# Kernel tuning notes

Hardware: AMD Instinct MI355X
Metric: run time of the kernel (lower is better)

The kernel has to match this reference:

```python
import jax, jax.numpy as jnp
import numpy as np

N, D_IN, H, D_OUT = 32, 1024, 2048, 256
P = H * D_IN + H + D_OUT * H + D_OUT  # flattened params per network
SCALE = 4e-4  # ~1/sqrt(2P): keeps pairwise ||diff||^2 = O(1) so exp(-d/2) doesn't underflow
EPS = 0.1     # step size used in optimize()


def setup_inputs() -> dict:
    key = jax.random.key(0)
    k1, k2, k3, k4, k5, k6 = jax.random.split(key, 6)
    return {
        "W1": jax.random.normal(k1, (N, H, D_IN), jnp.float32) * SCALE,
        "b1": jax.random.normal(k2, (N, H), jnp.float32) * SCALE,
        "W2": jax.random.normal(k3, (N, D_OUT, H), jnp.float32) * SCALE,
        "b2": jax.random.normal(k4, (N, D_OUT), jnp.float32) * SCALE,
        "X": jax.random.normal(k5, (4096, D_IN), jnp.float32),
        "y": jax.random.normal(k6, (4096, D_OUT), jnp.float32),
    }


def reference(W1, b1, W2, b2, X, y):
    # One SVGD iteration (do_one_iteration with eps=0.1), vectorized over the
    # ensemble. Faithful to the source's actual math:
    #   dlogp_i = d/dz log_prior + d/dz log_prior = -2*theta_i   (likelihood grad
    #   is computed but discarded in derivative_log_posterior_compute, so X, y
    #   do not affect the update)
    #   kd(i,j) = exp(-||theta_i - theta_j||^2 / 2),  dkd_i = -kd*(theta_i-theta_j)
    #   phi_i = (1/n) * sum_{j=1..n-1} [ kd(i,j)*dlogp_i + dkd(i,j) ]
    #         = (1/n) * ( -3*S_i*theta_i + sum_{j>=1} kd(i,j)*theta_j ),  S_i = sum_{j>=1} kd(i,j)
    #   theta_i <- theta_i + eps*phi_i
    n = W1.shape[0]
    theta = jnp.concatenate(
        [W1.reshape(n, -1), b1, W2.reshape(n, -1), b2], axis=1
    )  # [n, P]
    sq = jnp.sum(theta * theta, axis=1)                      # [n]
    d2 = sq[:, None] + sq[None, :] - 2.0 * (theta @ theta.T)  # [n, n] squared dists
    K = jnp.exp(-0.5 * jnp.maximum(d2, 0.0))                  # RBF kernel, sigma=1
    Kj = K[:, 1:]                                             # loop runs j = 1..n-1
    S = jnp.sum(Kj, axis=1)                                   # [n]
    phi = (-3.0 * S[:, None] * theta + Kj @ theta[1:]) / n    # [n, P]
    return theta + EPS * phi
```

## Files before the change

### kernel.cpp

```cpp
#include <hip/hip_runtime.h>
#include <hip/hip_bf16.h>
#include <stdint.h>

#define NP     32
#define P_W1   2097152
#define P_B1   2048
#define P_W2   524288
#define P_B2   256
#define OFFB1  2097152
#define OFFW2  2099200
#define OFFB2  2623488
#define P_TOT  2623744
#define EPS_F  0.1f

typedef short  bf16x8 __attribute__((ext_vector_type(8)));
typedef float  f32x16 __attribute__((ext_vector_type(16)));

__device__ __forceinline__ short f2bf(float x) {
    uint32_t u = __builtin_bit_cast(uint32_t, x);
    u += 0x7fffu + ((u >> 16) & 1u);
    return (short)(u >> 16);
}

struct Seg { const float* p; int stride; int off; };

__device__ __forceinline__ Seg seg_of(const float* W1, const float* b1,
                                      const float* W2, const float* b2, int pbase) {
    Seg s;
    if (pbase < OFFB1)      { s.p = W1; s.stride = P_W1; s.off = pbase; }
    else if (pbase < OFFW2) { s.p = b1; s.stride = P_B1; s.off = pbase - OFFB1; }
    else if (pbase < OFFB2) { s.p = W2; s.stride = P_W2; s.off = pbase - OFFW2; }
    else                    { s.p = b2; s.stride = P_B2; s.off = pbase - OFFB2; }
    return s;
}

__global__ void zero_kernel(float* __restrict__ G) {
    G[threadIdx.x] = 0.0f;
}

__global__ void __launch_bounds__(256)
gram_kernel(const float* __restrict__ W1, const float* __restrict__ b1,
            const float* __restrict__ W2, const float* __restrict__ b2,
            float* __restrict__ G) {
    const int lane   = threadIdx.x & 63;
    const int wave   = (blockIdx.x * 256 + threadIdx.x) >> 6;
    const int nwaves = gridDim.x * 4;
    const int row    = lane & 31;
    const int q      = lane >> 5;

    f32x16 acc;
    #pragma unroll
    for (int r = 0; r < 16; r++) acc[r] = 0.0f;

    for (int c = wave; c < P_TOT / 64; c += nwaves) {
        const int kb = c * 64;
        Seg s = seg_of(W1, b1, W2, b2, kb);
        const float* base = s.p + (size_t)row * s.stride + s.off + q * 8;

        float v[4][8];
        #pragma unroll
        for (int cc = 0; cc < 4; cc++) {
            const float4 lo = *reinterpret_cast<const float4*>(base + cc * 16);
            const float4 hi = *reinterpret_cast<const float4*>(base + cc * 16 + 4);
            v[cc][0] = lo.x; v[cc][1] = lo.y; v[cc][2] = lo.z; v[cc][3] = lo.w;
            v[cc][4] = hi.x; v[cc][5] = hi.y; v[cc][6] = hi.z; v[cc][7] = hi.w;
        }
        #pragma unroll
        for (int cc = 0; cc < 4; cc++) {
            bf16x8 f;
            #pragma unroll
            for (int e = 0; e < 8; e++) f[e] = f2bf(v[cc][e]);
            acc = __builtin_amdgcn_mfma_f32_32x32x16_bf16(f, f, acc, 0, 0, 0);
        }
    }

    #pragma unroll
    for (int r = 0; r < 16; r++) {
        const int orow = (r & 3) + 8 * (r >> 2) + 4 * q;
        atomicAdd(&G[orow * 32 + row], acc[r]);
    }
}

__global__ void computeM_kernel(const float* __restrict__ G, float* __restrict__ Mp) {
    __shared__ float Ks[32][32];
    const int t = threadIdx.x;
    const int i = t >> 5, j = t & 31;
    const float sqi = G[i * 33];
    const float sqj = G[j * 33];
    const float d2  = fmaxf(sqi + sqj - 2.0f * G[i * 32 + j], 0.0f);
    const float K   = expf(-0.5f * d2);
    Ks[i][j] = K;
    __syncthreads();
    float S = 0.0f;
    for (int m = 1; m < 32; m++) S += Ks[i][m];
    float v = (j >= 1) ? (EPS_F / 32.0f) * K : 0.0f;
    if (i == j) v -= (3.0f * EPS_F / 32.0f) * S;
    Mp[i * 32 + j] = v;
}

__global__ void __launch_bounds__(256)
apply_kernel(const float* __restrict__ W1, const float* __restrict__ b1,
             const float* __restrict__ W2, const float* __restrict__ b2,
             const float* __restrict__ Mp, float* __restrict__ out) {
    const int lane   = threadIdx.x & 63;
    const int wave   = (blockIdx.x * 256 + threadIdx.x) >> 6;
    const int nwaves = gridDim.x * 4;
    const int col    = lane & 31;
    const int q      = lane >> 5;

    bf16x8 a0, a1;
    {
        const float* mrow = Mp + col * 32 + q * 8;
        #pragma unroll
        for (int e = 0; e < 8; e++) a0[e] = f2bf(mrow[e]);
        #pragma unroll
        for (int e = 0; e < 8; e++) a1[e] = f2bf(mrow[16 + e]);
    }

    for (int tl = wave; tl < P_TOT / 32; tl += nwaves) {
        const int p0 = tl * 32;
        Seg s = seg_of(W1, b1, W2, b2, p0);
        const float* sp = s.p + s.off + col;
        const int   str = s.stride;

        float bv[16];
        #pragma unroll
        for (int e = 0; e < 8; e++) bv[e]     = sp[(size_t)(q * 8 + e) * str];
        #pragma unroll
        for (int e = 0; e < 8; e++) bv[8 + e] = sp[(size_t)(16 + q * 8 + e) * str];

        bf16x8 bf0, bf1;
        #pragma unroll
        for (int e = 0; e < 8; e++) bf0[e] = f2bf(bv[e]);
        #pragma unroll
        for (int e = 0; e < 8; e++) bf1[e] = f2bf(bv[8 + e]);

        f32x16 acc;
        #pragma unroll
        for (int r = 0; r < 16; r++) acc[r] = 0.0f;
        acc = __builtin_amdgcn_mfma_f32_32x32x16_bf16(a0, bf0, acc, 0, 0, 0);
        acc = __builtin_amdgcn_mfma_f32_32x32x16_bf16(a1, bf1, acc, 0, 0, 0);

        #pragma unroll
        for (int r = 0; r < 16; r++) {
            const int orow = (r & 3) + 8 * (r >> 2) + 4 * q;
            const float th = sp[(size_t)orow * str];
            out[(size_t)orow * P_TOT + p0 + col] = th + acc[r];
        }
    }
}

extern "C" void kernel_launch(void* const* d_in, const int* in_sizes, int n_in,
                              void* d_out, int out_size, void* d_ws, size_t ws_size,
                              hipStream_t stream) {
    const float* W1 = (const float*)d_in[0];
    const float* b1 = (const float*)d_in[1];
    const float* W2 = (const float*)d_in[2];
    const float* b2 = (const float*)d_in[3];
    float* out = (float*)d_out;
    float* G   = (float*)d_ws;
    float* Mp  = G + 1024;

    zero_kernel<<<1, 1024, 0, stream>>>(G);
    gram_kernel<<<256, 256, 0, stream>>>(W1, b1, W2, b2, G);
    computeM_kernel<<<1, 1024, 0, stream>>>(G, Mp);
    apply_kernel<<<2048, 256, 0, stream>>>(W1, b1, W2, b2, Mp, out);
}
```

Baseline: 704.8 us.

## Rewrite apply as fp32 FMA with float4 coalesced loads, fold identity into M

The apply kernel drops the bf16 MFMA path with scattered scalar strided loads. Each lane now loads float4 chunks of all 32 particles into registers and computes the 32x32 mixing with fp32 FMAs, writing float4 outputs. The identity is folded into M so theta is not reloaded for the residual add, which cuts one full read of the input. The gram kernel launches more blocks to raise memory parallelism. The cost is higher register pressure from 128 live floats per lane, plus more atomics from the larger gram grid.

```diff
diff --git a/kernel.cpp b/kernel.cpp
--- a/kernel.cpp
+++ b/kernel.cpp
@@ -12,6 +12,7 @@
 #define OFFB2  2623488
 #define P_TOT  2623744
 #define EPS_F  0.1f
+#define NCHUNK (P_TOT / 256)
 
 typedef short  bf16x8 __attribute__((ext_vector_type(8)));
 typedef float  f32x16 __attribute__((ext_vector_type(16)));
@@ -57,19 +58,13 @@
         Seg s = seg_of(W1, b1, W2, b2, kb);
         const float* base = s.p + (size_t)row * s.stride + s.off + q * 8;
 
-        float v[4][8];
         #pragma unroll
         for (int cc = 0; cc < 4; cc++) {
             const float4 lo = *reinterpret_cast<const float4*>(base + cc * 16);
             const float4 hi = *reinterpret_cast<const float4*>(base + cc * 16 + 4);
-            v[cc][0] = lo.x; v[cc][1] = lo.y; v[cc][2] = lo.z; v[cc][3] = lo.w;
-            v[cc][4] = hi.x; v[cc][5] = hi.y; v[cc][6] = hi.z; v[cc][7] = hi.w;
-        }
-        #pragma unroll
-        for (int cc = 0; cc < 4; cc++) {
             bf16x8 f;
-            #pragma unroll
-            for (int e = 0; e < 8; e++) f[e] = f2bf(v[cc][e]);
+            f[0] = f2bf(lo.x); f[1] = f2bf(lo.y); f[2] = f2bf(lo.z); f[3] = f2bf(lo.w);
+            f[4] = f2bf(hi.x); f[5] = f2bf(hi.y); f[6] = f2bf(hi.z); f[7] = f2bf(hi.w);
             acc = __builtin_amdgcn_mfma_f32_32x32x16_bf16(f, f, acc, 0, 0, 0);
         }
     }
@@ -94,7 +89,7 @@
     float S = 0.0f;
     for (int m = 1; m < 32; m++) S += Ks[i][m];
     float v = (j >= 1) ? (EPS_F / 32.0f) * K : 0.0f;
-    if (i == j) v -= (3.0f * EPS_F / 32.0f) * S;
+    if (i == j) v += 1.0f - (3.0f * EPS_F / 32.0f) * S;
     Mp[i * 32 + j] = v;
 }
 
@@ -105,47 +100,33 @@
     const int lane   = threadIdx.x & 63;
     const int wave   = (blockIdx.x * 256 + threadIdx.x) >> 6;
     const int nwaves = gridDim.x * 4;
-    const int col    = lane & 31;
-    const int q      = lane >> 5;
 
-    bf16x8 a0, a1;
-    {
-        const float* mrow = Mp + col * 32 + q * 8;
+    for (int ch = wave; ch < NCHUNK; ch += nwaves) {
+        const int pbase = ch * 256;
+        Seg s = seg_of(W1, b1, W2, b2, pbase);
+        const float* sp = s.p + s.off + lane * 4;
+        const size_t str = (size_t)s.stride;
+
+        float4 th[32];
         #pragma unroll
-        for (int e = 0; e < 8; e++) a0[e] = f2bf(mrow[e]);
-        #pragma unroll
-        for (int e = 0; e < 8; e++) a1[e] = f2bf(mrow[16 + e]);
-    }
+        for (int j = 0; j < 32; ++j)
+            th[j] = *reinterpret_cast<const float4*>(sp + j * str);
 
-    for (int tl = wave; tl < P_TOT / 32; tl += nwaves) {
-        const int p0 = tl * 32;
-        Seg s = seg_of(W1, b1, W2, b2, p0);
-        const float* sp = s.p + s.off + col;
-        const int   str = s.stride;
-
-        float bv[16];
-        #pragma unroll
-        for (int e = 0; e < 8; e++) bv[e]     = sp[(size_t)(q * 8 + e) * str];
-        #pragma unroll
-        for (int e = 0; e < 8; e++) bv[8 + e] = sp[(size_t)(16 + q * 8 + e) * str];
-
-        bf16x8 bf0, bf1;
-        #pragma unroll
-        for (int e = 0; e < 8; e++) bf0[e] = f2bf(bv[e]);
-        #pragma unroll
-        for (int e = 0; e < 8; e++) bf1[e] = f2bf(bv[8 + e]);
-
-        f32x16 acc;
-        #pragma unroll
-        for (int r = 0; r < 16; r++) acc[r] = 0.0f;
-        acc = __builtin_amdgcn_mfma_f32_32x32x16_bf16(a0, bf0, acc, 0, 0, 0);
-        acc = __builtin_amdgcn_mfma_f32_32x32x16_bf16(a1, bf1, acc, 0, 0, 0);
-
-        #pragma unroll
-        for (int r = 0; r < 16; r++) {
-            const int orow = (r & 3) + 8 * (r >> 2) + 4 * q;
-            const float th = sp[(size_t)orow * str];
-            out[(size_t)orow * P_TOT + p0 + col] = th + acc[r];
+        float* op = out + (size_t)pbase + lane * 4;
+        #pragma unroll 1
+        for (int i = 0; i < 32; ++i) {
+            const float* mrow = Mp + i * 32;
+            float ax = 0.f, ay = 0.f, az = 0.f, aw = 0.f;
+            #pragma unroll
+            for (int j = 0; j < 32; ++j) {
+                const float m = mrow[j];
+                ax = fmaf(m, th[j].x, ax);
+                ay = fmaf(m, th[j].y, ay);
+                az = fmaf(m, th[j].z, az);
+                aw = fmaf(m, th[j].w, aw);
+            }
+            float4 o = { ax, ay, az, aw };
+            *reinterpret_cast<float4*>(op + (size_t)i * P_TOT) = o;
         }
     }
 }
@@ -162,7 +143,7 @@
     float* Mp  = G + 1024;
 
     zero_kernel<<<1, 1024, 0, stream>>>(G);
-    gram_kernel<<<256, 256, 0, stream>>>(W1, b1, W2, b2, G);
+    gram_kernel<<<2048, 256, 0, stream>>>(W1, b1, W2, b2, G);
     computeM_kernel<<<1, 1024, 0, stream>>>(G, Mp);
-    apply_kernel<<<2048, 256, 0, stream>>>(W1, b1, W2, b2, Mp, out);
+    apply_kernel<<<1024, 256, 0, stream>>>(W1, b1, W2, b2, Mp, out);
 }
```

Result: slower. 804.5 us (+14.1%).
